# Kernel tuning notes

Hardware: AMD Instinct MI355X
Metric: run time of the kernel (lower is better)

Reference implementation:

```python
import jax, jax.numpy as jnp
import numpy as np

N, CIN, C, COUT, K27, KNN_K = 65536, 1, 128, 128, 27, 16
C4, C2 = C // 4, C // 2


def _w(key, shape, fan_in):
    return (jax.random.normal(key, shape, dtype=jnp.float32) * (fan_in ** -0.5))


def setup_inputs() -> dict:
    key = jax.random.key(0)
    ks = jax.random.split(key, 32)
    inp = {
        "feats": jax.random.normal(ks[0], (N, CIN), dtype=jnp.float32),
        # kernel-map neighbor indices; value N means 'no neighbor at this offset'
        "nbr_idx": jax.random.randint(ks[1], (N, K27), 0, N + 1, dtype=jnp.int32),
        "knn_idx": jax.random.randint(ks[2], (N, KNN_K), 0, N, dtype=jnp.int32),
        "W_in": _w(ks[3], (K27, CIN, C), K27 * CIN), "b_in": jnp.zeros((C,), jnp.float32),
        "W_conv0": _w(ks[4], (3, K27, C, C), K27 * C), "b_conv0": jnp.zeros((3, C), jnp.float32),
        "W_conv1": _w(ks[5], (3, K27, C, C), K27 * C), "b_conv1": jnp.zeros((3, C), jnp.float32),
        "Wq": _w(ks[6], (3, C, C), C), "Wk": _w(ks[7], (3, C, C), C),
        "Wv": _w(ks[8], (3, C, C), C), "Wo": _w(ks[9], (3, C, C), C),
        "bo": jnp.zeros((3, C), jnp.float32),
        "W_a0": _w(ks[10], (3, C, C4), C), "b_a0": jnp.zeros((3, C4), jnp.float32),
        "W_a1": _w(ks[11], (3, K27, C4, C4), K27 * C4), "b_a1": jnp.zeros((3, C4), jnp.float32),
        "W_a2": _w(ks[12], (3, C4, C2), C4), "b_a2": jnp.zeros((3, C2), jnp.float32),
        "W_b0": _w(ks[13], (3, K27, C, C4), K27 * C), "b_b0": jnp.zeros((3, C4), jnp.float32),
        "W_b1": _w(ks[14], (3, K27, C4, C2), K27 * C4), "b_b1": jnp.zeros((3, C2), jnp.float32),
        "W_out": _w(ks[15], (K27, C, COUT), K27 * C), "b_out": jnp.zeros((COUT,), jnp.float32),
    }
    return inp


def sparse_conv(x, idx, W, b):
    # x: [N,Cin]; idx: [N,27] with pad value N -> zero feature
    xp = jnp.concatenate([x, jnp.zeros((1, x.shape[1]), x.dtype)], axis=0)
    g = xp[idx]  # [N,27,Cin]
    return jnp.einsum('nkc,kco->no', g, W) + b


def knn_attn(x, idx, Wq, Wk, Wv, Wo, bo):
    q = x @ Wq
    kf = x @ Wk
    vf = x @ Wv
    kn = kf[idx]  # [N,k,C]
    vn = vf[idx]
    logits = jnp.einsum('nc,nkc->nk', q, kn) * (x.shape[-1] ** -0.5)
    a = jax.nn.softmax(logits, axis=-1)
    agg = jnp.einsum('nk,nkc->nc', a, vn)
    return x + agg @ Wo + bo


def irn(x, idx, Wa0, ba0, Wa1, ba1, Wa2, ba2, Wb0, bb0, Wb1, bb1):
    r = jax.nn.relu
    h = r(x @ Wa0 + ba0)                      # 1x1 conv
    h = r(sparse_conv(h, idx, Wa1, ba1))       # 3x3x3
    out0 = r(h @ Wa2 + ba2)                    # 1x1 conv
    g = r(sparse_conv(x, idx, Wb0, bb0))
    out1 = r(sparse_conv(g, idx, Wb1, bb1))
    return jnp.concatenate([out0, out1], axis=-1) + x


def reference(feats, nbr_idx, knn_idx, W_in, b_in, W_conv0, b_conv0, W_conv1, b_conv1,
              Wq, Wk, Wv, Wo, bo, W_a0, b_a0, W_a1, b_a1, W_a2, b_a2,
              W_b0, b_b0, W_b1, b_b1, W_out, b_out):
    r = jax.nn.relu
    out = sparse_conv(feats, nbr_idx, W_in, b_in)
    for s in range(3):
        h = sparse_conv(out, nbr_idx, W_conv0[s], b_conv0[s])
        h = r(knn_attn(h, knn_idx, Wq[s], Wk[s], Wv[s], Wo[s], bo[s]))
        h = sparse_conv(h, nbr_idx, W_conv1[s], b_conv1[s])
        out = irn(h, nbr_idx, W_a0[s], b_a0[s], W_a1[s], b_a1[s], W_a2[s], b_a2[s],
                  W_b0[s], b_b0[s], W_b1[s], b_b1[s])
    return sparse_conv(out, nbr_idx, W_out, b_out)
```

## Files before the change

kernel.cpp:

```cpp
#include <hip/hip_runtime.h>
#include <stdint.h>

typedef unsigned short u16;
typedef __attribute__((ext_vector_type(8))) short bf16x8;
typedef __attribute__((ext_vector_type(4))) float f32x4;

#define NPTS 65536
#define NK27 27
#define KNN 16

__device__ __forceinline__ u16 f2b(float f) {
  union { float f; uint32_t u; } v; v.f = f;
  uint32_t r = (v.u + 0x7fffu + ((v.u >> 16) & 1u)) >> 16;
  return (u16)r;
}
__device__ __forceinline__ float b2f(u16 h) {
  union { uint32_t u; float f; } v; v.u = ((uint32_t)h) << 16; return v.f;
}

template<int N>
__device__ __forceinline__ void waitcnt_vm() {
  __builtin_amdgcn_s_waitcnt((N & 0xF) | ((N >> 4) << 14) | (0x7 << 4) | (0xF << 8));
}

__global__ __launch_bounds__(256) void wtrans(const float* __restrict__ src, u16* __restrict__ dst,
                                              int G, int CI, int CO) {
  int id = blockIdx.x * 256 + threadIdx.x;
  int tot = G * CI * CO;
  if (id >= tot) return;
  int cpr = CI / 8;
  int swzb = (cpr < 8 ? cpr : 8) - 1;
  int g = id / (CI * CO);
  int r = id - g * (CI * CO);
  int co = r / CI;
  int cis = r - co * CI;
  int c = cis / 8, e = cis - c * 8;
  int ci = (c ^ (co & swzb)) * 8 + e;
  dst[id] = f2b(src[(size_t)g * CI * CO + (size_t)ci * CO + co]);
}

__global__ __launch_bounds__(256) void wtrans_in(const float* __restrict__ W, u16* __restrict__ dst) {
  int id = blockIdx.x * 256 + threadIdx.x;
  if (id >= 128 * 32) return;
  int co = id >> 5, cis = id & 31;
  int c = cis >> 3, e = cis & 7;
  int ci = ((c ^ (co & 3)) << 3) | e;
  dst[id] = (ci < NK27) ? f2b(W[ci * 128 + co]) : (u16)0;
}

__global__ __launch_bounds__(256) void g27(const float* __restrict__ feats, const int* __restrict__ nbr,
                                           u16* __restrict__ G) {
  int id = blockIdx.x * 256 + threadIdx.x;
  int n = id >> 5, j = id & 31;
  u16 v = 0;
  if (j < NK27) {
    int m = nbr[n * NK27 + j];
    if (m < NPTS) v = f2b(feats[m]);
  }
  G[id] = v;
}

__global__ __launch_bounds__(256) void itrans(const int* __restrict__ nbr, int* __restrict__ out) {
  int id = blockIdx.x * 256 + threadIdx.x;
  int k = id >> 16;
  int n = id & (NPTS - 1);
  out[id] = nbr[n * NK27 + k];
}

__global__ void zero_pads(u16* a, u16* b, u16* c, u16* d, u16* e) {
  int t = threadIdx.x;
  if (t < 128) { a[t] = 0; b[t] = 0; c[t] = 0; }
  if (t < 32) { d[t] = 0; e[t] = 0; }
}

#define GLDS16(g, l)                                                                        \
  __builtin_amdgcn_global_load_lds((const __attribute__((address_space(1))) void*)(g),      \
                                   (__attribute__((address_space(3))) void*)(l), 16, 0, 0)

template<int CIN, int COUT, int NK, int EMODE, bool OUTF32>
__global__ __launch_bounds__(512, 2)
void sconv(const u16* __restrict__ x, const int* __restrict__ idxt,
           const u16* __restrict__ Wt, const float* __restrict__ bias,
           const u16* __restrict__ res, int res_stride,
           void* __restrict__ yout, int out_stride) {
  static_assert(NK == 1 || ((NK - 1) % 2 == 0), "NK odd or 1");
  constexpr int BM = 256;
  constexpr int KK = CIN / 32;
  constexpr int CPR = CIN / 8;
  constexpr int SWZB = (CPR < 8 ? CPR : 8) - 1;
  constexpr int N_REP = COUT / 16;
  constexpr int M_REP = 2;
  constexpr int BSZ = COUT * CIN;
  constexpr int BCH = BSZ / 8;
  constexpr int BISS = (BCH + 511) / 512;
  constexpr int AC = M_REP * KK;
  constexpr int IC = M_REP;
  constexpr int VC_F = AC + IC;
  constexpr int VC_L = AC;

  __shared__ __attribute__((aligned(16))) u16 Bs[2][BSZ];

  const int tid = threadIdx.x;
  const int lane = tid & 63;
  const int wave = tid >> 6;
  const int n0 = blockIdx.x * BM;
  const int lr = lane & 15;
  const int lh = lane >> 4;
  const int row0 = wave * 32;

  f32x4 acc[M_REP][N_REP];
#pragma unroll
  for (int i = 0; i < M_REP; ++i)
#pragma unroll
    for (int j = 0; j < N_REP; ++j) acc[i][j] = (f32x4){0.f, 0.f, 0.f, 0.f};

  bf16x8 A0[M_REP][KK], A1[M_REP][KK];
  int mna[M_REP], mnb[M_REP];

  auto stageB = [&](int k, u16* dst) {
    const u16* src = Wt + (size_t)k * BSZ;
#pragma unroll
    for (int i = 0; i < BISS; ++i) {
      int cb = i * 512 + wave * 64;
      if (BCH % 512 == 0 || cb < BCH)
        GLDS16(src + (size_t)(cb + lane) * 8, dst + (size_t)cb * 8);
    }
  };
  auto loadIdx = [&](int k, int (&m)[M_REP]) {
#pragma unroll
    for (int mr = 0; mr < M_REP; ++mr)
      m[mr] = idxt[(size_t)k * NPTS + n0 + row0 + mr * 16 + lr];
  };
  auto issueA = [&](const int (&m)[M_REP], bf16x8 (&dst)[M_REP][KK]) {
#pragma unroll
    for (int mr = 0; mr < M_REP; ++mr)
#pragma unroll
      for (int kk = 0; kk < KK; ++kk)
        dst[mr][kk] = *(const bf16x8*)(x + (size_t)m[mr] * CIN + kk * 32 + lh * 8);
  };
  auto compute = [&](const u16* bsp, const bf16x8 (&AR)[M_REP][KK]) {
#pragma unroll
    for (int kk = 0; kk < KK; ++kk) {
      bf16x8 b[N_REP];
      int pc = (kk * 4 + lh) ^ (lr & SWZB);
#pragma unroll
      for (int nr = 0; nr < N_REP; ++nr)
        b[nr] = *(const bf16x8*)(bsp + (size_t)(nr * 16 + lr) * CIN + pc * 8);
#pragma unroll
      for (int mr = 0; mr < M_REP; ++mr)
#pragma unroll
        for (int nr = 0; nr < N_REP; ++nr)
          acc[mr][nr] = __builtin_amdgcn_mfma_f32_16x16x32_bf16(AR[mr][kk], b[nr], acc[mr][nr], 0, 0, 0);
    }
  };

  if constexpr (NK == 1) {
    int m0[M_REP];
#pragma unroll
    for (int mr = 0; mr < M_REP; ++mr) m0[mr] = n0 + row0 + mr * 16 + lr;
    stageB(0, &Bs[0][0]);
    issueA(m0, A0);
    __syncthreads();
    compute(&Bs[0][0], A0);
  } else {
    int m0[M_REP];
    loadIdx(0, m0);
    __builtin_amdgcn_sched_barrier(0);
    stageB(0, &Bs[0][0]);
    __builtin_amdgcn_sched_barrier(0);
    issueA(m0, A0);
    __builtin_amdgcn_sched_barrier(0);
    loadIdx(1, mnb);
    __builtin_amdgcn_sched_barrier(0);

#define TAPX(kv, P, ACUR, ANXT, MUSE, MWRT)                                   \
    {                                                                         \
      const int k_ = (kv);                                                    \
      __builtin_amdgcn_sched_barrier(0);                                      \
      waitcnt_vm<VC_F>();                                                     \
      __builtin_amdgcn_s_barrier();                                           \
      __builtin_amdgcn_sched_barrier(0);                                      \
      stageB(k_ + 1, &Bs[(P) ^ 1][0]);                                        \
      __builtin_amdgcn_sched_barrier(0);                                      \
      issueA(MUSE, ANXT);                                                     \
      __builtin_amdgcn_sched_barrier(0);                                      \
      if (k_ + 2 < NK) loadIdx(k_ + 2, MWRT);                                 \
      __builtin_amdgcn_sched_barrier(0);                                      \
      compute(&Bs[P][0], ACUR);                                               \
    }

    for (int k = 0; k < NK - 1; k += 2) {
      TAPX(k, 0, A0, A1, mnb, mna);
      TAPX(k + 1, 1, A1, A0, mna, mnb);
    }
#undef TAPX
    __builtin_amdgcn_sched_barrier(0);
    waitcnt_vm<VC_L>();
    __builtin_amdgcn_s_barrier();
    __builtin_amdgcn_sched_barrier(0);
    compute(&Bs[0][0], A0);
  }

#pragma unroll
  for (int mr = 0; mr < M_REP; ++mr) {
#pragma unroll
    for (int nr = 0; nr < N_REP; ++nr) {
      int col = nr * 16 + lr;
      float bv = bias ? bias[col] : 0.0f;
#pragma unroll
      for (int j = 0; j < 4; ++j) {
        int n = n0 + row0 + mr * 16 + lh * 4 + j;
        float v = acc[mr][nr][j] + bv;
        if (EMODE == 1) v = fmaxf(v, 0.0f);
        else if (EMODE == 2) v = fmaxf(v + b2f(res[(size_t)n * res_stride + col]), 0.0f);
        else if (EMODE == 3) v = fmaxf(v, 0.0f) + b2f(res[(size_t)n * res_stride + col]);
        if (OUTF32) ((float*)yout)[(size_t)n * out_stride + col] = v;
        else ((u16*)yout)[(size_t)n * out_stride + col] = f2b(v);
      }
    }
  }
}

__global__ __launch_bounds__(512, 2)
void qkv_k(const u16* __restrict__ x, const u16* __restrict__ Wt,
           u16* __restrict__ qo, u16* __restrict__ ko, u16* __restrict__ vo) {
  constexpr int CIN = 128, COUT = 128;
  constexpr int KK = 4, SWZB = 7, N_REP = 8, M_REP = 2;
  constexpr int BSZ = COUT * CIN;
  constexpr int BISS = (BSZ / 8) / 512;

  __shared__ __attribute__((aligned(16))) u16 Bs[BSZ];

  const int tid = threadIdx.x;
  const int lane = tid & 63;
  const int wave = tid >> 6;
  const int n0 = blockIdx.x * 256;
  const int lr = lane & 15;
  const int lh = lane >> 4;
  const int row0 = wave * 32;

  bf16x8 A0[M_REP][KK];
#pragma unroll
  for (int mr = 0; mr < M_REP; ++mr)
#pragma unroll
    for (int kk = 0; kk < KK; ++kk)
      A0[mr][kk] = *(const bf16x8*)(x + (size_t)(n0 + row0 + mr * 16 + lr) * CIN + kk * 32 + lh * 8);

  u16* outs[3] = {qo, ko, vo};
  for (int w = 0; w < 3; ++w) {
    if (w) __syncthreads();
    const u16* src = Wt + (size_t)w * BSZ;
#pragma unroll
    for (int i = 0; i < BISS; ++i) {
      int cb = i * 512 + wave * 64;
      GLDS16(src + (size_t)(cb + lane) * 8, &Bs[(size_t)cb * 8]);
    }
    __syncthreads();

    f32x4 acc[M_REP][N_REP];
#pragma unroll
    for (int i = 0; i < M_REP; ++i)
#pragma unroll
      for (int j = 0; j < N_REP; ++j) acc[i][j] = (f32x4){0.f, 0.f, 0.f, 0.f};
#pragma unroll
    for (int kk = 0; kk < KK; ++kk) {
      bf16x8 b[N_REP];
      int pc = (kk * 4 + lh) ^ (lr & SWZB);
#pragma unroll
      for (int nr = 0; nr < N_REP; ++nr)
        b[nr] = *(const bf16x8*)(&Bs[(size_t)(nr * 16 + lr) * CIN + pc * 8]);
#pragma unroll
      for (int mr = 0; mr < M_REP; ++mr)
#pragma unroll
        for (int nr = 0; nr < N_REP; ++nr)
          acc[mr][nr] = __builtin_amdgcn_mfma_f32_16x16x32_bf16(A0[mr][kk], b[nr], acc[mr][nr], 0, 0, 0);
    }
    u16* yo = outs[w];
#pragma unroll
    for (int mr = 0; mr < M_REP; ++mr)
#pragma unroll
      for (int nr = 0; nr < N_REP; ++nr) {
        int col = nr * 16 + lr;
#pragma unroll
        for (int j = 0; j < 4; ++j) {
          int n = n0 + row0 + mr * 16 + lh * 4 + j;
          yo[(size_t)n * 128 + col] = f2b(acc[mr][nr][j]);
        }
      }
  }
}

__global__ __launch_bounds__(256)
void attn_k(const u16* __restrict__ qb, const u16* __restrict__ kb,
            const u16* __restrict__ vb, const int* __restrict__ knn,
            u16* __restrict__ agg) {
  const int t = blockIdx.x * 256 + threadIdx.x;
  const int n = t >> 4;
  const int s = t & 15;
  const int lane = threadIdx.x & 63;
  const int gbase = lane & 48;

  int myidx = knn[n * KNN + s];

  bf16x8 q8 = *(const bf16x8*)(qb + (size_t)n * 128 + s * 8);
  float qf[8];
#pragma unroll
  for (int c = 0; c < 4; ++c) {
    uint32_t u = ((const uint32_t*)&q8)[c];
    qf[2 * c] = b2f((u16)(u & 0xffff));
    qf[2 * c + 1] = b2f((u16)(u >> 16));
  }

  float lg[KNN];
  int ms[KNN];
#pragma unroll
  for (int j = 0; j < KNN; ++j) {
    int mj = __shfl(myidx, gbase | j);
    ms[j] = mj;
    bf16x8 k8 = *(const bf16x8*)(kb + (size_t)mj * 128 + s * 8);
    float d = 0.f;
#pragma unroll
    for (int c = 0; c < 4; ++c) {
      uint32_t u = ((const uint32_t*)&k8)[c];
      d += qf[2 * c] * b2f((u16)(u & 0xffff));
      d += qf[2 * c + 1] * b2f((u16)(u >> 16));
    }
    d += __shfl_xor(d, 1);
    d += __shfl_xor(d, 2);
    d += __shfl_xor(d, 4);
    d += __shfl_xor(d, 8);
    lg[j] = d * 0.08838834764831845f;
  }
  float mx = lg[0];
#pragma unroll
  for (int j = 1; j < KNN; ++j) mx = fmaxf(mx, lg[j]);
  float ssum = 0.f;
#pragma unroll
  for (int j = 0; j < KNN; ++j) { lg[j] = __expf(lg[j] - mx); ssum += lg[j]; }
  float inv = 1.0f / ssum;

  float a[8] = {0, 0, 0, 0, 0, 0, 0, 0};
#pragma unroll
  for (int j = 0; j < KNN; ++j) {
    bf16x8 v8 = *(const bf16x8*)(vb + (size_t)ms[j] * 128 + s * 8);
    float w = lg[j];
#pragma unroll
    for (int c = 0; c < 4; ++c) {
      uint32_t u = ((const uint32_t*)&v8)[c];
      a[2 * c] += w * b2f((u16)(u & 0xffff));
      a[2 * c + 1] += w * b2f((u16)(u >> 16));
    }
  }
  uint32_t ow[4];
#pragma unroll
  for (int c = 0; c < 4; ++c)
    ow[c] = (uint32_t)f2b(a[2 * c] * inv) | ((uint32_t)f2b(a[2 * c + 1] * inv) << 16);
  *(uint32_t*)(agg + (size_t)n * 128 + s * 8 + 0) = ow[0];
  *(uint32_t*)(agg + (size_t)n * 128 + s * 8 + 2) = ow[1];
  *(uint32_t*)(agg + (size_t)n * 128 + s * 8 + 4) = ow[2];
  *(uint32_t*)(agg + (size_t)n * 128 + s * 8 + 6) = ow[3];
}

extern "C" void kernel_launch(void* const* d_in, const int* in_sizes, int n_in,
                              void* d_out, int out_size, void* d_ws, size_t ws_size,
                              hipStream_t stream) {
  (void)in_sizes; (void)n_in; (void)out_size; (void)ws_size;
  const float* feats = (const float*)d_in[0];
  const int*   nbr   = (const int*)d_in[1];
  const int*   knn   = (const int*)d_in[2];
  const float* W_in  = (const float*)d_in[3];
  const float* b_in  = (const float*)d_in[4];
  const float* W_c0  = (const float*)d_in[5];
  const float* b_c0  = (const float*)d_in[6];
  const float* W_c1  = (const float*)d_in[7];
  const float* b_c1  = (const float*)d_in[8];
  const float* Wq    = (const float*)d_in[9];
  const float* Wk    = (const float*)d_in[10];
  const float* Wv    = (const float*)d_in[11];
  const float* Wo    = (const float*)d_in[12];
  const float* bo    = (const float*)d_in[13];
  const float* Wa0   = (const float*)d_in[14];
  const float* ba0   = (const float*)d_in[15];
  const float* Wa1   = (const float*)d_in[16];
  const float* ba1   = (const float*)d_in[17];
  const float* Wa2   = (const float*)d_in[18];
  const float* ba2   = (const float*)d_in[19];
  const float* Wb0   = (const float*)d_in[20];
  const float* bb0   = (const float*)d_in[21];
  const float* Wb1   = (const float*)d_in[22];
  const float* bb1   = (const float*)d_in[23];
  const float* W_out = (const float*)d_in[24];
  const float* b_out = (const float*)d_in[25];

  char* ws = (char*)d_ws;
  size_t off = 0;
  auto alloc = [&](size_t bytes) { size_t r = off; off += (bytes + 255) & ~(size_t)255; return r; };

  u16* wt_c0  = (u16*)(ws + alloc((size_t)81 * 16384 * 2));
  u16* wt_c1  = (u16*)(ws + alloc((size_t)81 * 16384 * 2));
  u16* wt_qkv = (u16*)(ws + alloc((size_t)9 * 16384 * 2));
  u16* wt_o   = (u16*)(ws + alloc((size_t)3 * 16384 * 2));
  u16* wt_a0  = (u16*)(ws + alloc((size_t)3 * 128 * 32 * 2));
  u16* wt_a1  = (u16*)(ws + alloc((size_t)81 * 32 * 32 * 2));
  u16* wt_a2  = (u16*)(ws + alloc((size_t)3 * 32 * 64 * 2));
  u16* wt_b0  = (u16*)(ws + alloc((size_t)81 * 128 * 32 * 2));
  u16* wt_b1  = (u16*)(ws + alloc((size_t)81 * 32 * 64 * 2));
  u16* wt_out = (u16*)(ws + alloc((size_t)27 * 16384 * 2));
  u16* wt_in  = (u16*)(ws + alloc((size_t)128 * 32 * 2));
  int* idx_t  = (int*)(ws + alloc((size_t)NK27 * NPTS * 4));
  u16* G27    = (u16*)(ws + alloc((size_t)NPTS * 32 * 2));

  u16* B0 = (u16*)(ws + alloc((size_t)(NPTS + 1) * 128 * 2));
  u16* B1 = (u16*)(ws + alloc((size_t)NPTS * 128 * 2));
  u16* KB = (u16*)(ws + alloc((size_t)(NPTS + 1) * 128 * 2));
  u16* VB = (u16*)(ws + alloc((size_t)(NPTS + 1) * 128 * 2));
  u16* QB = (u16*)(ws + alloc((size_t)NPTS * 128 * 2));
  u16* H1 = (u16*)(ws + alloc((size_t)(NPTS + 1) * 32 * 2));
  u16* HA = (u16*)(ws + alloc((size_t)NPTS * 32 * 2));
  u16* G  = (u16*)(ws + alloc((size_t)(NPTS + 1) * 32 * 2));
  u16* AGG = B0;
  u16* B2 = KB;
  u16* B3 = VB;

  auto TG = [](int tot) { return (tot + 255) / 256; };
  wtrans<<<TG(81 * 16384), 256, 0, stream>>>(W_c0, wt_c0, 81, 128, 128);
  wtrans<<<TG(81 * 16384), 256, 0, stream>>>(W_c1, wt_c1, 81, 128, 128);
  wtrans<<<TG(16384), 256, 0, stream>>>(Wq + 0 * 16384, wt_qkv + (size_t)0 * 16384, 1, 128, 128);
  wtrans<<<TG(16384), 256, 0, stream>>>(Wk + 0 * 16384, wt_qkv + (size_t)1 * 16384, 1, 128, 128);
  wtrans<<<TG(16384), 256, 0, stream>>>(Wv + 0 * 16384, wt_qkv + (size_t)2 * 16384, 1, 128, 128);
  wtrans<<<TG(16384), 256, 0, stream>>>(Wq + 1 * 16384, wt_qkv + (size_t)3 * 16384, 1, 128, 128);
  wtrans<<<TG(16384), 256, 0, stream>>>(Wk + 1 * 16384, wt_qkv + (size_t)4 * 16384, 1, 128, 128);
  wtrans<<<TG(16384), 256, 0, stream>>>(Wv + 1 * 16384, wt_qkv + (size_t)5 * 16384, 1, 128, 128);
  wtrans<<<TG(16384), 256, 0, stream>>>(Wq + 2 * 16384, wt_qkv + (size_t)6 * 16384, 1, 128, 128);
  wtrans<<<TG(16384), 256, 0, stream>>>(Wk + 2 * 16384, wt_qkv + (size_t)7 * 16384, 1, 128, 128);
  wtrans<<<TG(16384), 256, 0, stream>>>(Wv + 2 * 16384, wt_qkv + (size_t)8 * 16384, 1, 128, 128);
  wtrans<<<TG(3 * 16384), 256, 0, stream>>>(Wo, wt_o, 3, 128, 128);
  wtrans<<<TG(3 * 128 * 32), 256, 0, stream>>>(Wa0, wt_a0, 3, 128, 32);
  wtrans<<<TG(81 * 32 * 32), 256, 0, stream>>>(Wa1, wt_a1, 81, 32, 32);
  wtrans<<<TG(3 * 32 * 64), 256, 0, stream>>>(Wa2, wt_a2, 3, 32, 64);
  wtrans<<<TG(81 * 128 * 32), 256, 0, stream>>>(Wb0, wt_b0, 81, 128, 32);
  wtrans<<<TG(81 * 32 * 64), 256, 0, stream>>>(Wb1, wt_b1, 81, 32, 64);
  wtrans<<<TG(27 * 16384), 256, 0, stream>>>(W_out, wt_out, 27, 128, 128);
  wtrans_in<<<TG(128 * 32), 256, 0, stream>>>(W_in, wt_in);
  itrans<<<NK27 * NPTS / 256, 256, 0, stream>>>(nbr, idx_t);

  zero_pads<<<1, 256, 0, stream>>>(B0 + (size_t)NPTS * 128, KB + (size_t)NPTS * 128,
                                   VB + (size_t)NPTS * 128, H1 + (size_t)NPTS * 32,
                                   G + (size_t)NPTS * 32);

  g27<<<NPTS * 32 / 256, 256, 0, stream>>>(feats, nbr, G27);
  sconv<32, 128, 1, 0, false><<<NPTS / 256, 512, 0, stream>>>(G27, nullptr, wt_in, b_in, nullptr, 0, B0, 128);

  const int GB = NPTS / 256;
  for (int s = 0; s < 3; ++s) {
    const u16* wc0 = wt_c0 + (size_t)s * 27 * 16384;
    const u16* wc1 = wt_c1 + (size_t)s * 27 * 16384;
    const u16* wqkv = wt_qkv + (size_t)s * 3 * 16384;
    const u16* wos = wt_o + (size_t)s * 16384;
    const u16* wa0 = wt_a0 + (size_t)s * 4096;
    const u16* wa1 = wt_a1 + (size_t)s * 27648;
    const u16* wa2 = wt_a2 + (size_t)s * 2048;
    const u16* wb0 = wt_b0 + (size_t)s * 110592;
    const u16* wb1 = wt_b1 + (size_t)s * 55296;

    sconv<128, 128, 27, 0, false><<<GB, 512, 0, stream>>>(B0, idx_t, wc0, b_c0 + s * 128, nullptr, 0, B1, 128);
    qkv_k<<<GB, 512, 0, stream>>>(B1, wqkv, QB, KB, VB);
    attn_k<<<NPTS / 16, 256, 0, stream>>>(QB, KB, VB, knn, AGG);
    sconv<128, 128, 1, 2, false><<<GB, 512, 0, stream>>>(AGG, nullptr, wos, bo + s * 128, B1, 128, B2, 128);
    sconv<128, 128, 27, 0, false><<<GB, 512, 0, stream>>>(B2, idx_t, wc1, b_c1 + s * 128, nullptr, 0, B3, 128);
    sconv<128, 32, 1, 1, false><<<GB, 512, 0, stream>>>(B3, nullptr, wa0, ba0 + s * 32, nullptr, 0, H1, 32);
    sconv<32, 32, 27, 1, false><<<GB, 512, 0, stream>>>(H1, idx_t, wa1, ba1 + s * 32, nullptr, 0, HA, 32);
    sconv<32, 64, 1, 3, false><<<GB, 512, 0, stream>>>(HA, idx_t, wa2, ba2 + s * 64, B3, 128, B0, 128);
    sconv<128, 32, 27, 1, false><<<GB, 512, 0, stream>>>(B3, idx_t, wb0, bb0 + s * 32, nullptr, 0, G, 32);
    sconv<32, 64, 27, 3, false><<<GB, 512, 0, stream>>>(G, idx_t, wb1, bb1 + s * 64, B3 + 64, 128, (void*)(B0 + 64), 128);
  }
  sconv<128, 128, 27, 0, true><<<GB, 512, 0, stream>>>(B0, idx_t, wt_out, b_out, nullptr, 0, d_out, 128);
}
```

Measured before the change: 1.204 ms.

## Deepen sparse-conv pipeline to process tap pairs with four LDS weight slabs

Restructures the 27-tap sparse convolution main loop to stage weights for two taps at a time into four LDS slabs and keep three register sets of gathered rows in flight. Each step now needs one barrier and waitcnt per pair of taps instead of one per tap, and the gather loads run further ahead of the MFMA work. The point is to hide gather and weight-load latency and cut synchronisation. In exchange it doubles LDS use for the 128x128 case, which can lower occupancy under launch_bounds(512,2), and it adds register pressure. The index buffer is enlarged so a prefetch of index row 27 stays in bounds.

```diff
diff --git a/kernel.cpp b/kernel.cpp
--- a/kernel.cpp
+++ b/kernel.cpp
@@ -83,7 +83,7 @@
            const u16* __restrict__ Wt, const float* __restrict__ bias,
            const u16* __restrict__ res, int res_stride,
            void* __restrict__ yout, int out_stride) {
-  static_assert(NK == 1 || ((NK - 1) % 2 == 0), "NK odd or 1");
+  static_assert(NK == 1 || NK == 27, "NK 1 or 27");
   constexpr int BM = 256;
   constexpr int KK = CIN / 32;
   constexpr int CPR = CIN / 8;
@@ -94,11 +94,12 @@
   constexpr int BCH = BSZ / 8;
   constexpr int BISS = (BCH + 511) / 512;
   constexpr int AC = M_REP * KK;
-  constexpr int IC = M_REP;
-  constexpr int VC_F = AC + IC;
+  constexpr int IC = 2 * M_REP;
+  constexpr int VC_E = 2 * AC + IC;
   constexpr int VC_L = AC;
-
-  __shared__ __attribute__((aligned(16))) u16 Bs[2][BSZ];
+  constexpr int NSLAB = (NK > 1) ? 4 : 1;
+
+  __shared__ __attribute__((aligned(16))) u16 Bs[NSLAB][BSZ];
 
   const int tid = threadIdx.x;
   const int lane = tid & 63;
@@ -114,11 +115,12 @@
 #pragma unroll
     for (int j = 0; j < N_REP; ++j) acc[i][j] = (f32x4){0.f, 0.f, 0.f, 0.f};
 
-  bf16x8 A0[M_REP][KK], A1[M_REP][KK];
-  int mna[M_REP], mnb[M_REP];
-
-  auto stageB = [&](int k, u16* dst) {
+  bf16x8 S0[M_REP][KK], S1[M_REP][KK], S2[M_REP][KK];
+  int I0[2][M_REP], I1[2][M_REP];
+
+  auto stage1 = [&](int k, int slab) {
     const u16* src = Wt + (size_t)k * BSZ;
+    u16* dst = &Bs[(NK > 1) ? slab : 0][0];
 #pragma unroll
     for (int i = 0; i < BISS; ++i) {
       int cb = i * 512 + wave * 64;
@@ -126,10 +128,12 @@
         GLDS16(src + (size_t)(cb + lane) * 8, dst + (size_t)cb * 8);
     }
   };
-  auto loadIdx = [&](int k, int (&m)[M_REP]) {
-#pragma unroll
-    for (int mr = 0; mr < M_REP; ++mr)
-      m[mr] = idxt[(size_t)k * NPTS + n0 + row0 + mr * 16 + lr];
+  auto loadIdxPair = [&](int p, int (&m)[2][M_REP]) {
+#pragma unroll
+    for (int t = 0; t < 2; ++t)
+#pragma unroll
+      for (int mr = 0; mr < M_REP; ++mr)
+        m[t][mr] = idxt[(size_t)(2 * p + t) * NPTS + n0 + row0 + mr * 16 + lr];
   };
   auto issueA = [&](const int (&m)[M_REP], bf16x8 (&dst)[M_REP][KK]) {
 #pragma unroll
@@ -138,7 +142,8 @@
       for (int kk = 0; kk < KK; ++kk)
         dst[mr][kk] = *(const bf16x8*)(x + (size_t)m[mr] * CIN + kk * 32 + lh * 8);
   };
-  auto compute = [&](const u16* bsp, const bf16x8 (&AR)[M_REP][KK]) {
+  auto compute = [&](int slab, const bf16x8 (&AR)[M_REP][KK]) {
+    const u16* bsp = &Bs[(NK > 1) ? slab : 0][0];
 #pragma unroll
     for (int kk = 0; kk < KK; ++kk) {
       bf16x8 b[N_REP];
@@ -154,52 +159,75 @@
     }
   };
 
+#define SBAR __builtin_amdgcn_sched_barrier(0)
+
   if constexpr (NK == 1) {
     int m0[M_REP];
 #pragma unroll
     for (int mr = 0; mr < M_REP; ++mr) m0[mr] = n0 + row0 + mr * 16 + lr;
-    stageB(0, &Bs[0][0]);
-    issueA(m0, A0);
+    stage1(0, 0);
+    issueA(m0, S0);
     __syncthreads();
-    compute(&Bs[0][0], A0);
+    compute(0, S0);
   } else {
-    int m0[M_REP];
-    loadIdx(0, m0);
-    __builtin_amdgcn_sched_barrier(0);
-    stageB(0, &Bs[0][0]);
-    __builtin_amdgcn_sched_barrier(0);
-    issueA(m0, A0);
-    __builtin_amdgcn_sched_barrier(0);
-    loadIdx(1, mnb);
-    __builtin_amdgcn_sched_barrier(0);
-
-#define TAPX(kv, P, ACUR, ANXT, MUSE, MWRT)                                   \
-    {                                                                         \
-      const int k_ = (kv);                                                    \
-      __builtin_amdgcn_sched_barrier(0);                                      \
-      waitcnt_vm<VC_F>();                                                     \
-      __builtin_amdgcn_s_barrier();                                           \
-      __builtin_amdgcn_sched_barrier(0);                                      \
-      stageB(k_ + 1, &Bs[(P) ^ 1][0]);                                        \
-      __builtin_amdgcn_sched_barrier(0);                                      \
-      issueA(MUSE, ANXT);                                                     \
-      __builtin_amdgcn_sched_barrier(0);                                      \
-      if (k_ + 2 < NK) loadIdx(k_ + 2, MWRT);                                 \
-      __builtin_amdgcn_sched_barrier(0);                                      \
-      compute(&Bs[P][0], ACUR);                                               \
-    }
-
-    for (int k = 0; k < NK - 1; k += 2) {
-      TAPX(k, 0, A0, A1, mnb, mna);
-      TAPX(k + 1, 1, A1, A0, mna, mnb);
-    }
-#undef TAPX
-    __builtin_amdgcn_sched_barrier(0);
+    loadIdxPair(0, I0);
+    SBAR;
+    stage1(0, 0); stage1(1, 1);
+    SBAR;
+    issueA(I0[0], S0);
+    SBAR;
+    issueA(I0[1], S1);
+    SBAR;
+    loadIdxPair(1, I1);
+    SBAR;
+
+#define PERX(p, SA, SB, SC, IU, IW, C0, C1, N0, N1)                           \
+    waitcnt_vm<VC_E>();                                                       \
+    __builtin_amdgcn_s_barrier();                                             \
+    SBAR;                                                                     \
+    stage1(2 * (p) + 2, N0);                                                  \
+    stage1(2 * (p) + 3, N1);                                                  \
+    SBAR;                                                                     \
+    issueA(IU[0], SC);                                                        \
+    SBAR;                                                                     \
+    loadIdxPair((p) + 2, IW);                                                 \
+    SBAR;                                                                     \
+    compute(C0, SA);                                                          \
+    SBAR;                                                                     \
+    issueA(IU[1], SA);                                                        \
+    SBAR;                                                                     \
+    compute(C1, SB);                                                          \
+    SBAR;
+
+#define SIXP(pb)                                                              \
+    PERX(pb + 0, S0, S1, S2, I1, I0, 0, 1, 2, 3)                              \
+    PERX(pb + 1, S2, S0, S1, I0, I1, 2, 3, 0, 1)                              \
+    PERX(pb + 2, S1, S2, S0, I1, I0, 0, 1, 2, 3)                              \
+    PERX(pb + 3, S0, S1, S2, I0, I1, 2, 3, 0, 1)                              \
+    PERX(pb + 4, S2, S0, S1, I1, I0, 0, 1, 2, 3)                              \
+    PERX(pb + 5, S1, S2, S0, I0, I1, 2, 3, 0, 1)
+
+    SIXP(0)
+    SIXP(6)
+    waitcnt_vm<VC_E>();
+    __builtin_amdgcn_s_barrier();
+    SBAR;
+    stage1(26, 2);
+    SBAR;
+    issueA(I1[0], S2);
+    SBAR;
+    compute(0, S0);
+    SBAR;
+    compute(1, S1);
+    SBAR;
     waitcnt_vm<VC_L>();
     __builtin_amdgcn_s_barrier();
-    __builtin_amdgcn_sched_barrier(0);
-    compute(&Bs[0][0], A0);
-  }
+    SBAR;
+    compute(2, S2);
+#undef SIXP
+#undef PERX
+  }
+#undef SBAR
 
 #pragma unroll
   for (int mr = 0; mr < M_REP; ++mr) {
@@ -407,7 +435,7 @@
   u16* wt_b1  = (u16*)(ws + alloc((size_t)81 * 32 * 64 * 2));
   u16* wt_out = (u16*)(ws + alloc((size_t)27 * 16384 * 2));
   u16* wt_in  = (u16*)(ws + alloc((size_t)128 * 32 * 2));
-  int* idx_t  = (int*)(ws + alloc((size_t)NK27 * NPTS * 4));
+  int* idx_t  = (int*)(ws + alloc((size_t)(NK27 + 1) * NPTS * 4));
   u16* G27    = (u16*)(ws + alloc((size_t)NPTS * 32 * 2));
 
   u16* B0 = (u16*)(ws + alloc((size_t)(NPTS + 1) * 128 * 2));
```

Result: no change. 1.182 ms (-1.9%).
